# Kernel optimization log

Hardware: AMD Instinct MI355X
Metric: run time of the kernel (lower is better)

Reference implementation:

```python
import jax, jax.numpy as jnp
import numpy as np
import jax.scipy.linalg as jsl

# ---- module constants (mirror __init__ buffers) ----
T0, T1, DT = 0.0, 1.0, 1e-3
DIM, NSTEPS, M, TQ, B = 8, 2048, 64, 1024, 1
DS = (T1 - T0) / NSTEPS
STEPS = jnp.linspace(T0, T1, NSTEPS + 1)            # [S+1]
ZPTS = jnp.linspace(T0 + DT * 5.5, T1 - DT * 5.5, M)  # inducing points [M]
SQRT_DS = float(np.sqrt(DS))
SQRT_DT = float(np.sqrt(DT))


def _hurst(t, y0, W1, b1, W2, b2, Wc1, bc1, Wc2, bc2, dw, cw):
    # compute_hurst: sigmoid(driving_action(t)*dw + condition_net(y0)*cw)
    tc_in = t.reshape(-1, 1)                                             # [N,1]
    feat = jnp.concatenate([jnp.sin(tc_in), jnp.cos(tc_in), tc_in], -1)  # [N,3]
    tc = jax.nn.sigmoid(jnp.tanh(feat @ W1.T + b1) @ W2.T + b2)          # [N,dim]
    pc = jax.nn.sigmoid(jnp.tanh(y0 @ Wc1.T + bc1) @ Wc2.T + bc2)        # [1,dim]
    return jax.nn.sigmoid(tc * dw + pc * cw)                             # [N,dim]


def _safe_pow(x, a):
    # x**a for x>=0, with well-defined (zero) gradient at x==0
    mask = x > 0
    xs = jnp.where(mask, x, 1.0)
    return jnp.where(mask, xs ** a, 0.0)


def _compute_weight(t, y0, params, eps=1e-12):
    # compute_weight (Muniandy et al. weight); returns [S, N, dim]
    h = _hurst(t, y0, *params)[None]                              # [1,N,dim]
    d0 = jax.nn.relu(t[None, :] - STEPS[:-1, None])[..., None]    # [S,N,1]
    d1 = jax.nn.relu(t[None, :] - STEPS[1:, None])[..., None]     # [S,N,1]
    w = jnp.sqrt(_safe_pow(d0, 2.0 * h) - _safe_pow(d1, 2.0 * h) + eps)
    w = w / jnp.sqrt(2.0 * h * DS)
    return w / jnp.exp(jax.lax.lgamma(h + 0.5))


def _increment_weight(t, y0, params):
    # increment_weight: g_i / dt (finite difference of clamped weights)
    wa = jnp.maximum(_compute_weight(t, y0, params), 0.0)
    wb = jnp.maximum(_compute_weight(t + DT, y0, params), 0.0)
    return jnp.maximum((wb - wa) * SQRT_DS / DT, 0.0)             # [S,N,dim]


def _forward(t, y0, eps_z, W1, b1, W2, b2, Wc1, bc1, Wc2, bc2, dw, cw):
    params = (W1, b1, W2, b2, Wc1, bc1, Wc2, bc2, dw, cw)
    # --- precompute (inducing points) ---
    Kz = _increment_weight(ZPTS, y0, params)                # [S,M,dim]
    Kzz = jnp.einsum('smd,skd->dmk', Kz, Kz)                # [dim,M,M]
    Lz = jnp.linalg.cholesky(Kzz + 1e-6 * jnp.eye(M, dtype=Kzz.dtype))
    delta_Bz = jnp.einsum('dmk,dkb->dmb', Lz, eps_z)        # [dim,M,B]
    # --- forward (mean / sqrt(var)*sqrt(dt)) ---
    Kt = _increment_weight(t, y0, params)                   # [S,T,dim]
    Ktz = jnp.einsum('std,smd->dtm', Kt, Kz)                # [dim,T,M]
    alpha = jax.vmap(lambda L, b: jsl.cho_solve((L, True), b))(
        Lz, jnp.swapaxes(Ktz, -1, -2))                      # [dim,M,T]
    mean = jnp.einsum('dmt,dmb->dtb', alpha, delta_Bz)      # [dim,T,B]
    Ktt = jnp.einsum('std,sud->dtu', Kt, Kt)                # [dim,T,T]
    var = Ktt - jnp.einsum('dmt,dmu->dtu', alpha, alpha)    # [dim,T,T]
    std = jnp.sqrt(jnp.maximum(var, 1e-12)) * SQRT_DT
    return mean.reshape(-1, DIM), std.reshape(-1, DIM)


def setup_inputs() -> dict:
    key = jax.random.key(0)
    ks = jax.random.split(key, 12)
    return {
        't': jax.random.uniform(ks[0], (TQ,), jnp.float32, T0 + 0.05, T1 - 0.05),
        'y0': jax.random.normal(ks[1], (1, 1), jnp.float32),
        'eps_z': jax.random.normal(ks[2], (DIM, M, B), jnp.float32),
        'W1': jax.random.normal(ks[3], (10, 3), jnp.float32) * 0.3,
        'b1': jax.random.normal(ks[4], (10,), jnp.float32) * 0.1,
        'W2': jax.random.normal(ks[5], (DIM, 10), jnp.float32) * 0.3,
        'b2': jax.random.normal(ks[6], (DIM,), jnp.float32) * 0.1,
        'Wc1': jax.random.normal(ks[7], (10, 1), jnp.float32) * 0.3,
        'bc1': jax.random.normal(ks[8], (10,), jnp.float32) * 0.1,
        'Wc2': jax.random.normal(ks[9], (DIM, 10), jnp.float32) * 0.3,
        'bc2': jax.random.normal(ks[10], (DIM,), jnp.float32) * 0.1,
        'dw': jnp.array([0.5], jnp.float32),
        'cw': jnp.array([0.5], jnp.float32),
    }


def reference(t, y0, eps_z, W1, b1, W2, b2, Wc1, bc1, Wc2, bc2, dw, cw):
    return _forward(t, y0, eps_z, W1, b1, W2, b2, Wc1, bc1, Wc2, bc2, dw, cw)
```

## Files before the change

### kernel.cpp

```cpp
#include <hip/hip_runtime.h>
#include <cmath>

#define DIMN 8
#define SSTEPS 2048
#define MZ 64
#define TQN 1024
#define DS_F    4.8828125e-4f
#define DT_F    1.0e-3f
#define SCALE_F 22.09708691207961f
#define SQRTDT_F 0.031622776601683794f
#define LN2_F   0.6931471805599453f

typedef _Float16 f16x8 __attribute__((ext_vector_type(8)));
typedef float f32x4 __attribute__((ext_vector_type(4)));

__device__ __forceinline__ float sigmoidf_(float x) { return 1.f / (1.f + expf(-x)); }

__device__ __forceinline__ void gl_lds16(const _Float16* g, _Float16* l)
{
    __builtin_amdgcn_global_load_lds(
        (const __attribute__((address_space(1))) unsigned int*)g,
        (__attribute__((address_space(3))) unsigned int*)l, 16, 0, 0);
}

__global__ void coef_kernel(const float* __restrict__ t_in, const float* __restrict__ y0,
                            const float* __restrict__ W1, const float* __restrict__ b1,
                            const float* __restrict__ W2, const float* __restrict__ b2,
                            const float* __restrict__ Wc1, const float* __restrict__ bc1,
                            const float* __restrict__ Wc2, const float* __restrict__ bc2,
                            const float* __restrict__ dw, const float* __restrict__ cw,
                            float4* __restrict__ coef_t, float4* __restrict__ coef_z,
                            float* __restrict__ times_z)
{
    int gid = blockIdx.x * blockDim.x + threadIdx.x;
    if (gid >= TQN + MZ) return;
    bool isz = gid >= TQN;
    float tv;
    if (!isz) {
        tv = t_in[gid];
    } else {
        int j = gid - TQN;
        tv = 0.0055f + (float)j * (0.989f / 63.0f);
        times_z[j] = tv;
    }
    float y = y0[0];
    float hc[10];
    #pragma unroll
    for (int j = 0; j < 10; ++j) hc[j] = tanhf(y * Wc1[j] + bc1[j]);
    float pc[DIMN];
    #pragma unroll
    for (int d = 0; d < DIMN; ++d) {
        float s = bc2[d];
        #pragma unroll
        for (int j = 0; j < 10; ++j) s += hc[j] * Wc2[d * 10 + j];
        pc[d] = sigmoidf_(s);
    }
    float dww = dw[0], cww = cw[0];
    float4 outv[DIMN];
    for (int which = 0; which < 2; ++which) {
        float tt = (which == 0) ? tv : tv + DT_F;
        float st = sinf(tt), ct = cosf(tt);
        float hid[10];
        #pragma unroll
        for (int j = 0; j < 10; ++j)
            hid[j] = tanhf(st * W1[j * 3 + 0] + ct * W1[j * 3 + 1] + tt * W1[j * 3 + 2] + b1[j]);
        #pragma unroll
        for (int d = 0; d < DIMN; ++d) {
            float s = b2[d];
            #pragma unroll
            for (int j = 0; j < 10; ++j) s += hid[j] * W2[d * 10 + j];
            float tc = sigmoidf_(s);
            float h = sigmoidf_(tc * dww + pc[d] * cww);
            float e = 2.f * h;
            float c = rsqrtf(e * DS_F) / tgammaf(h + 0.5f);
            if (which == 0) { outv[d].x = e; outv[d].y = c; }
            else            { outv[d].z = e; outv[d].w = c; }
        }
    }
    float4* dst = isz ? (coef_z + (size_t)(gid - TQN) * DIMN) : (coef_t + (size_t)gid * DIMN);
    #pragma unroll
    for (int d = 0; d < DIMN; ++d) dst[d] = outv[d];
}

__device__ __forceinline__ void side_weights(float tt, float e, float c, int sbase,
                                             float (&w)[8])
{
    float xprev = tt - (float)sbase * DS_F;
    float pa = 0.f;
    if (xprev > 0.f) pa = __builtin_amdgcn_exp2f(e * __builtin_amdgcn_logf(xprev));
    #pragma unroll
    for (int k = 1; k <= 8; ++k) {
        float xk = tt - (float)(sbase + k) * DS_F;
        float D, pan;
        if (xk > 0.f) {
            float om = xk * __builtin_amdgcn_rcpf(xprev);
            float y2 = e * __builtin_amdgcn_logf(om);
            float wl = y2 * LN2_F;
            float em = wl * (1.f + wl * (0.5f + wl * (0.16666667f + wl * (0.041666668f + wl * 0.008333334f))));
            float g = -em;
            if (wl < -0.3f) g = 1.f - __builtin_amdgcn_exp2f(y2);
            D = pa * g;
            pan = pa - D;
        } else {
            D = pa;
            pan = 0.f;
        }
        w[k - 1] = __builtin_amdgcn_sqrtf(D + 1e-12f) * c;
        pa = pan;
        xprev = xk;
    }
}

__device__ __forceinline__ unsigned pack_hl(float v)
{
    _Float16 h = (_Float16)v;
    _Float16 l = (_Float16)(v - (float)h);
    unsigned short hu = __builtin_bit_cast(unsigned short, h);
    unsigned short lu = __builtin_bit_cast(unsigned short, l);
    return (unsigned)hu | ((unsigned)lu << 16);
}

__global__ __launch_bounds__(256) void kmat_t_kernel(const float* __restrict__ times,
                                                     const float4* __restrict__ coef,
                                                     _Float16* __restrict__ KThi,
                                                     _Float16* __restrict__ KTlo)
{
    int tid = threadIdx.x;
    int txx = tid & 31, sidx = tid >> 5;
    int t = blockIdx.x * 32 + txx;
    int sbase = blockIdx.y * 64 + sidx * 8;
    int d = blockIdx.z;
    __shared__ unsigned shhl[32][65];
    float tq = times[t];
    float4 cf = coef[(size_t)t * DIMN + d];
    float wa[8], wb[8];
    side_weights(tq,        cf.x, cf.y, sbase, wa);
    side_weights(tq + DT_F, cf.z, cf.w, sbase, wb);
    #pragma unroll
    for (int k = 0; k < 8; ++k) {
        float v = fmaxf(wb[k] - wa[k], 0.f) * SCALE_F;
        shhl[txx][sidx * 8 + k] = pack_hl(v);
    }
    __syncthreads();
    int tl = tid >> 3, sc = tid & 7;
    unsigned dwv[8];
    #pragma unroll
    for (int j = 0; j < 8; ++j) dwv[j] = shhl[tl][sc * 8 + j];
    uint4 hv, lv;
    hv.x = __builtin_amdgcn_perm(dwv[1], dwv[0], 0x05040100u);
    hv.y = __builtin_amdgcn_perm(dwv[3], dwv[2], 0x05040100u);
    hv.z = __builtin_amdgcn_perm(dwv[5], dwv[4], 0x05040100u);
    hv.w = __builtin_amdgcn_perm(dwv[7], dwv[6], 0x05040100u);
    lv.x = __builtin_amdgcn_perm(dwv[1], dwv[0], 0x07060302u);
    lv.y = __builtin_amdgcn_perm(dwv[3], dwv[2], 0x07060302u);
    lv.z = __builtin_amdgcn_perm(dwv[5], dwv[4], 0x07060302u);
    lv.w = __builtin_amdgcn_perm(dwv[7], dwv[6], 0x07060302u);
    size_t o = ((size_t)(d * 1024) + blockIdx.x * 32 + tl) * 2048 + blockIdx.y * 64 + sc * 8;
    *(uint4*)&KThi[o] = hv;
    *(uint4*)&KTlo[o] = lv;
}

__global__ __launch_bounds__(256) void kmat_z_kernel(const float* __restrict__ times,
                                                     const float4* __restrict__ coef,
                                                     float* __restrict__ Kz,
                                                     _Float16* __restrict__ KzThi,
                                                     _Float16* __restrict__ KzTlo)
{
    int tid = threadIdx.x;
    int txx = tid & 31, sidx = tid >> 5;
    int m = blockIdx.x * 32 + txx;
    int sbase = blockIdx.y * 64 + sidx * 8;
    int d = blockIdx.z;
    __shared__ unsigned shhl[32][65];
    float tq = times[m];
    float4 cf = coef[(size_t)m * DIMN + d];
    float wa[8], wb[8];
    side_weights(tq,        cf.x, cf.y, sbase, wa);
    side_weights(tq + DT_F, cf.z, cf.w, sbase, wb);
    #pragma unroll
    for (int k = 0; k < 8; ++k) {
        float v = fmaxf(wb[k] - wa[k], 0.f) * SCALE_F;
        Kz[((size_t)d * SSTEPS + sbase + k) * 64 + m] = v;
        shhl[txx][sidx * 8 + k] = pack_hl(v);
    }
    __syncthreads();
    int tl = tid >> 3, sc = tid & 7;
    unsigned dwv[8];
    #pragma unroll
    for (int j = 0; j < 8; ++j) dwv[j] = shhl[tl][sc * 8 + j];
    uint4 hv, lv;
    hv.x = __builtin_amdgcn_perm(dwv[1], dwv[0], 0x05040100u);
    hv.y = __builtin_amdgcn_perm(dwv[3], dwv[2], 0x05040100u);
    hv.z = __builtin_amdgcn_perm(dwv[5], dwv[4], 0x05040100u);
    hv.w = __builtin_amdgcn_perm(dwv[7], dwv[6], 0x05040100u);
    lv.x = __builtin_amdgcn_perm(dwv[1], dwv[0], 0x07060302u);
    lv.y = __builtin_amdgcn_perm(dwv[3], dwv[2], 0x07060302u);
    lv.z = __builtin_amdgcn_perm(dwv[5], dwv[4], 0x07060302u);
    lv.w = __builtin_amdgcn_perm(dwv[7], dwv[6], 0x07060302u);
    size_t o = ((size_t)(d * 64) + blockIdx.x * 32 + tl) * 2048 + blockIdx.y * 64 + sc * 8;
    *(uint4*)&KzThi[o] = hv;
    *(uint4*)&KzTlo[o] = lv;
}

__global__ __launch_bounds__(256) void kzz_partial_kernel(const float* __restrict__ Kz,
                                                          float* __restrict__ part)
{
    int kidx = blockIdx.x;
    int d = blockIdx.y;
    int tid = threadIdx.x, tx = tid & 15, ty = tid >> 4;
    __shared__ float As[32][64];
    float acc[4][4] = {};
    const float* base = Kz + ((size_t)d * SSTEPS + (size_t)kidx * 256) * 64;
    for (int c = 0; c < 8; ++c) {
        __syncthreads();
        #pragma unroll
        for (int l = 0; l < 2; ++l) {
            int idx = tid + l * 256;
            int r = idx >> 4, c4 = idx & 15;
            *(float4*)&As[r][c4 * 4] = *(const float4*)(base + (size_t)(c * 32 + r) * 64 + c4 * 4);
        }
        __syncthreads();
        #pragma unroll
        for (int k = 0; k < 32; ++k) {
            float av[4], bv[4];
            *(float4*)&av[0] = *(float4*)&As[k][ty * 4];
            *(float4*)&bv[0] = *(float4*)&As[k][tx * 4];
            #pragma unroll
            for (int i = 0; i < 4; ++i)
                #pragma unroll
                for (int j = 0; j < 4; ++j) acc[i][j] += av[i] * bv[j];
        }
    }
    float* dst = part + (size_t)(kidx * DIMN + d) * 4096;
    #pragma unroll
    for (int i = 0; i < 4; ++i)
        *(float4*)&dst[(size_t)(ty * 4 + i) * 64 + tx * 4] =
            make_float4(acc[i][0], acc[i][1], acc[i][2], acc[i][3]);
}

__global__ void reduce_kernel(const float* __restrict__ in, float* __restrict__ out,
                              int n, int parts)
{
    int i = blockIdx.x * 256 + threadIdx.x;
    if (i >= n) return;
    float s = 0.f;
    for (int p = 0; p < parts; ++p) s += in[(size_t)p * n + i];
    out[i] = s;
}

__global__ __launch_bounds__(64) void chol_kernel(const float* __restrict__ Kzz,
                                                  const float* __restrict__ eps_z,
                                                  float* __restrict__ Lz, float* __restrict__ dBz)
{
    int d = blockIdx.x, i = threadIdx.x;
    __shared__ float A[64][65];
    for (int r = 0; r < 64; ++r)
        A[r][i] = Kzz[(size_t)d * 4096 + (size_t)r * 64 + i] + ((r == i) ? 1e-6f : 0.f);
    __syncthreads();
    for (int j = 0; j < 64; ++j) {
        float s = 0.f;
        if (i >= j) {
            s = A[i][j];
            for (int k = 0; k < j; ++k) s -= A[i][k] * A[j][k];
        }
        __syncthreads();
        if (i == j) A[j][j] = sqrtf(fmaxf(s, 1e-30f));
        __syncthreads();
        if (i > j) A[i][j] = s / A[j][j];
        __syncthreads();
    }
    for (int r = 0; r < 64; ++r)
        Lz[(size_t)d * 4096 + (size_t)r * 64 + i] = (i <= r) ? A[r][i] : 0.f;
    float s = 0.f;
    for (int k = 0; k <= i; ++k) s += A[i][k] * eps_z[d * 64 + k];
    dBz[d * 64 + i] = s;
}

__global__ __launch_bounds__(256, 2) void ktz_mfma_kernel(const _Float16* __restrict__ KThi,
                                                          const _Float16* __restrict__ KTlo,
                                                          const _Float16* __restrict__ KzThi,
                                                          const _Float16* __restrict__ KzTlo,
                                                          float* __restrict__ part)
{
    int tid = threadIdx.x;
    int wave = tid >> 6, lane = tid & 63;
    int n = lane & 15, q = lane >> 4;
    int lr = lane >> 2, lc = (lane & 3) * 8;
    int d = blockIdx.x;
    int t0 = blockIdx.y * 128;
    int split = blockIdx.z;
    int wr = (wave >> 1) * 64, wc = (wave & 1) * 32;

    __shared__ _Float16 Ah[2][128][32], Al[2][128][32];
    __shared__ _Float16 Bh[2][64][32],  Bl[2][64][32];

    f32x4 acc[4][2];
    #pragma unroll
    for (int i = 0; i < 4; ++i)
        #pragma unroll
        for (int j = 0; j < 2; ++j) acc[i][j] = (f32x4)0.f;

    const size_t aRow = (size_t)(d * 1024 + t0);
    const size_t bRow = (size_t)(d * 64);
    int segA = wave * 32;
    int segB = wave * 16;

    auto stage = [&](int buf, int c) {
        int s0 = split * 512 + c * 32;
        size_t ga = (aRow + segA + lr) * 2048 + s0 + lc;
        size_t gb = (bRow + segB + lr) * 2048 + s0 + lc;
        gl_lds16(KThi + ga,               &Ah[buf][segA][0]);
        gl_lds16(KThi + ga + 16 * 2048,   &Ah[buf][segA + 16][0]);
        gl_lds16(KTlo + ga,               &Al[buf][segA][0]);
        gl_lds16(KTlo + ga + 16 * 2048,   &Al[buf][segA + 16][0]);
        gl_lds16(KzThi + gb,              &Bh[buf][segB][0]);
        gl_lds16(KzTlo + gb,              &Bl[buf][segB][0]);
    };

    stage(0, 0);
    __syncthreads();
    for (int c = 0; c < 16; ++c) {
        int buf = c & 1;
        if (c + 1 < 16) stage(buf ^ 1, c + 1);
        f16x8 fAh[4], fAl[4], fBh[2], fBl[2];
        #pragma unroll
        for (int i = 0; i < 4; ++i) {
            fAh[i] = *(f16x8*)&Ah[buf][wr + i * 16 + n][q * 8];
            fAl[i] = *(f16x8*)&Al[buf][wr + i * 16 + n][q * 8];
        }
        #pragma unroll
        for (int j = 0; j < 2; ++j) {
            fBh[j] = *(f16x8*)&Bh[buf][wc + j * 16 + n][q * 8];
            fBl[j] = *(f16x8*)&Bl[buf][wc + j * 16 + n][q * 8];
        }
        #pragma unroll
        for (int i = 0; i < 4; ++i)
            #pragma unroll
            for (int j = 0; j < 2; ++j) {
                acc[i][j] = __builtin_amdgcn_mfma_f32_16x16x32_f16(fAh[i], fBh[j], acc[i][j], 0, 0, 0);
                acc[i][j] = __builtin_amdgcn_mfma_f32_16x16x32_f16(fAh[i], fBl[j], acc[i][j], 0, 0, 0);
                acc[i][j] = __builtin_amdgcn_mfma_f32_16x16x32_f16(fAl[i], fBh[j], acc[i][j], 0, 0, 0);
            }
        __syncthreads();
    }
    float* dst = part + ((size_t)(split * DIMN + d)) * 1024 * 64;
    #pragma unroll
    for (int i = 0; i < 4; ++i)
        #pragma unroll
        for (int j = 0; j < 2; ++j)
            #pragma unroll
            for (int r = 0; r < 4; ++r) {
                int t = t0 + wr + i * 16 + q * 4 + r;
                dst[(size_t)t * 64 + wc + j * 16 + n] = acc[i][j][r];
            }
}

__global__ __launch_bounds__(64) void solve_kernel(const float* __restrict__ Lz,
                                                   const float* __restrict__ part2,
                                                   const float* __restrict__ dBz,
                                                   _Float16* __restrict__ aPhi,
                                                   _Float16* __restrict__ aPlo,
                                                   _Float16* __restrict__ aNhi,
                                                   _Float16* __restrict__ aNlo,
                                                   float* __restrict__ out0)
{
    int d = blockIdx.y;
    int t0 = blockIdx.x * 64;
    int i = threadIdx.x;
    __shared__ float L[64][65];
    __shared__ float bL[64][65];
    __shared__ float inv[64];
    __shared__ float dB[64];
    for (int r = 0; r < 64; ++r)
        L[r][i] = Lz[(size_t)d * 4096 + (size_t)r * 64 + i];
    dB[i] = dBz[d * 64 + i];
    for (int r = 0; r < 64; ++r) {
        size_t base = ((size_t)d * 1024 + t0 + r) * 64 + i;
        float s = part2[base] + part2[base + 524288] + part2[base + 1048576] + part2[base + 1572864];
        bL[i][r] = s;
    }
    __syncthreads();
    inv[i] = 1.f / L[i][i];
    __syncthreads();
    for (int j = 0; j < 64; ++j) {
        float s = bL[j][i];
        for (int k = 0; k < j; ++k) s -= L[j][k] * bL[k][i];
        bL[j][i] = s * inv[j];
    }
    for (int j = 63; j >= 0; --j) {
        float s = bL[j][i];
        for (int k = j + 1; k < 64; ++k) s -= L[k][j] * bL[k][i];
        bL[j][i] = s * inv[j];
    }
    float mn = 0.f;
    for (int m = 0; m < 64; ++m) mn += bL[m][i] * dB[m];
    out0[d * 1024 + t0 + i] = mn;
    size_t o = ((size_t)(d * 1024 + t0 + i)) * 64;
    for (int g = 0; g < 8; ++g) {
        union { _Float16 h[8]; float4 v; } ph, pl, nh, nl;
        #pragma unroll
        for (int k = 0; k < 8; ++k) {
            float x = bL[g * 8 + k][i];
            _Float16 h = (_Float16)x;
            _Float16 lo = (_Float16)(x - (float)h);
            ph.h[k] = h;  pl.h[k] = lo;
            nh.h[k] = -h; nl.h[k] = -lo;
        }
        *(float4*)&aPhi[o + g * 8] = ph.v;
        *(float4*)&aPlo[o + g * 8] = pl.v;
        *(float4*)&aNhi[o + g * 8] = nh.v;
        *(float4*)&aNlo[o + g * 8] = nl.v;
    }
}

__global__ __launch_bounds__(256, 2) void var_mfma_kernel(const _Float16* __restrict__ KThi,
                                                          const _Float16* __restrict__ KTlo,
                                                          const _Float16* __restrict__ aPhi,
                                                          const _Float16* __restrict__ aPlo,
                                                          const _Float16* __restrict__ aNhi,
                                                          const _Float16* __restrict__ aNlo,
                                                          float* __restrict__ out1)
{
    int tid = threadIdx.x;
    int wave = tid >> 6, lane = tid & 63;
    int n = lane & 15, q = lane >> 4;
    int lr = lane >> 2, lc = (lane & 3) * 8;
    int d = blockIdx.x;
    int t0 = blockIdx.y * 128, u0 = blockIdx.z * 128;
    int wr = (wave >> 1) * 64, wc = (wave & 1) * 64;

    __shared__ _Float16 Ah[2][128][32], Al[2][128][32], Bh[2][128][32], Bl[2][128][32];

    f32x4 acc[4][4];
    #pragma unroll
    for (int i = 0; i < 4; ++i)
        #pragma unroll
        for (int j = 0; j < 4; ++j) acc[i][j] = (f32x4)0.f;

    const size_t aRow = (size_t)(d * 1024 + t0);
    const size_t bRow = (size_t)(d * 1024 + u0);
    int segA = wave * 32;

    auto stage = [&](int buf, int ck) {
        const _Float16 *ph, *pl, *qh, *ql;
        size_t str; int col;
        if (ck < 64) { ph = KThi; pl = KTlo; qh = KThi; ql = KTlo; str = 2048; col = ck * 32; }
        else         { ph = aPhi; pl = aPlo; qh = aNhi; ql = aNlo; str = 64;  col = (ck - 64) * 32; }
        size_t ga = (aRow + segA + lr) * str + col + lc;
        size_t gb = (bRow + segA + lr) * str + col + lc;
        gl_lds16(ph + ga,            &Ah[buf][segA][0]);
        gl_lds16(ph + ga + 16 * str, &Ah[buf][segA + 16][0]);
        gl_lds16(pl + ga,            &Al[buf][segA][0]);
        gl_lds16(pl + ga + 16 * str, &Al[buf][segA + 16][0]);
        gl_lds16(qh + gb,            &Bh[buf][segA][0]);
        gl_lds16(qh + gb + 16 * str, &Bh[buf][segA + 16][0]);
        gl_lds16(ql + gb,            &Bl[buf][segA][0]);
        gl_lds16(ql + gb + 16 * str, &Bl[buf][segA + 16][0]);
    };

    stage(0, 0);
    __syncthreads();
    for (int ck = 0; ck < 66; ++ck) {
        int buf = ck & 1;
        if (ck + 1 < 66) stage(buf ^ 1, ck + 1);
        f16x8 fAh[4], fAl[4], fBh[4], fBl[4];
        #pragma unroll
        for (int i = 0; i < 4; ++i) {
            fAh[i] = *(f16x8*)&Ah[buf][wr + i * 16 + n][q * 8];
            fAl[i] = *(f16x8*)&Al[buf][wr + i * 16 + n][q * 8];
            fBh[i] = *(f16x8*)&Bh[buf][wc + i * 16 + n][q * 8];
            fBl[i] = *(f16x8*)&Bl[buf][wc + i * 16 + n][q * 8];
        }
        #pragma unroll
        for (int i = 0; i < 4; ++i)
            #pragma unroll
            for (int j = 0; j < 4; ++j) {
                acc[i][j] = __builtin_amdgcn_mfma_f32_16x16x32_f16(fAh[i], fBh[j], acc[i][j], 0, 0, 0);
                acc[i][j] = __builtin_amdgcn_mfma_f32_16x16x32_f16(fAh[i], fBl[j], acc[i][j], 0, 0, 0);
                acc[i][j] = __builtin_amdgcn_mfma_f32_16x16x32_f16(fAl[i], fBh[j], acc[i][j], 0, 0, 0);
            }
        __syncthreads();
    }
    float* dst = out1 + ((size_t)d << 20);
    #pragma unroll
    for (int i = 0; i < 4; ++i)
        #pragma unroll
        for (int j = 0; j < 4; ++j)
            #pragma unroll
            for (int r = 0; r < 4; ++r) {
                int t = t0 + wr + i * 16 + q * 4 + r;
                int u = u0 + wc + j * 16 + n;
                float v = acc[i][j][r];
                dst[(size_t)t * 1024 + u] = sqrtf(fmaxf(v, 1e-12f)) * SQRTDT_F;
            }
}

extern "C" void kernel_launch(void* const* d_in, const int* in_sizes, int n_in,
                              void* d_out, int out_size, void* d_ws, size_t ws_size,
                              hipStream_t stream)
{
    const float* t_in  = (const float*)d_in[0];
    const float* y0    = (const float*)d_in[1];
    const float* eps_z = (const float*)d_in[2];
    const float* W1    = (const float*)d_in[3];
    const float* b1    = (const float*)d_in[4];
    const float* W2    = (const float*)d_in[5];
    const float* b2    = (const float*)d_in[6];
    const float* Wc1   = (const float*)d_in[7];
    const float* bc1   = (const float*)d_in[8];
    const float* Wc2   = (const float*)d_in[9];
    const float* bc2   = (const float*)d_in[10];
    const float* dw    = (const float*)d_in[11];
    const float* cw    = (const float*)d_in[12];

    float* ws = (float*)d_ws;
    size_t off = 0;
    auto carve = [&](size_t n) { float* p = ws + off; off += n; return p; };
    float* coef_t   = carve(32768);
    float* coef_z   = carve(2048);
    float* times_z  = carve(64);
    float* Kzz      = carve(32768);
    float* Lz       = carve(32768);
    float* dBz      = carve(512);
    float* Kz       = carve(1048576);
    _Float16* KThi  = (_Float16*)carve(8388608);
    _Float16* KTlo  = (_Float16*)carve(8388608);
    _Float16* KzThi = (_Float16*)carve(524288);
    _Float16* KzTlo = (_Float16*)carve(524288);
    float* part1    = carve(262144);
    float* part2    = carve(2097152);
    _Float16* aPhi  = (_Float16*)carve(262144);
    _Float16* aPlo  = (_Float16*)carve(262144);
    _Float16* aNhi  = (_Float16*)carve(262144);
    _Float16* aNlo  = (_Float16*)carve(262144);

    float* out0 = (float*)d_out;
    float* out1 = out0 + (size_t)DIMN * 1024;

    coef_kernel<<<9, 128, 0, stream>>>(t_in, y0, W1, b1, W2, b2, Wc1, bc1, Wc2, bc2, dw, cw,
                                       (float4*)coef_t, (float4*)coef_z, times_z);
    kmat_t_kernel<<<dim3(32, 32, 8), 256, 0, stream>>>(t_in, (const float4*)coef_t,
                                                       KThi, KTlo);
    kmat_z_kernel<<<dim3(2, 32, 8), 256, 0, stream>>>(times_z, (const float4*)coef_z,
                                                      Kz, KzThi, KzTlo);
    kzz_partial_kernel<<<dim3(8, 8), 256, 0, stream>>>(Kz, part1);
    reduce_kernel<<<128, 256, 0, stream>>>(part1, Kzz, 32768, 8);
    chol_kernel<<<8, 64, 0, stream>>>(Kzz, eps_z, Lz, dBz);
    ktz_mfma_kernel<<<dim3(8, 8, 4), 256, 0, stream>>>(KThi, KTlo, KzThi, KzTlo, part2);
    solve_kernel<<<dim3(16, 8), 64, 0, stream>>>(Lz, part2, dBz, aPhi, aPlo, aNhi, aNlo, out0);
    var_mfma_kernel<<<dim3(8, 8, 8), 256, 0, stream>>>(KThi, KTlo, aPhi, aPlo, aNhi, aNlo, out1);
}
```

Baseline: 385.9 us.

## Skip zero weight strips, drop LDS transpose, load MFMA B operands directly to registers

```diff
diff --git a/kernel.cpp b/kernel.cpp
--- a/kernel.cpp
+++ b/kernel.cpp
@@ -111,53 +111,37 @@
     }
 }
 
-__device__ __forceinline__ unsigned pack_hl(float v)
-{
-    _Float16 h = (_Float16)v;
-    _Float16 l = (_Float16)(v - (float)h);
-    unsigned short hu = __builtin_bit_cast(unsigned short, h);
-    unsigned short lu = __builtin_bit_cast(unsigned short, l);
-    return (unsigned)hu | ((unsigned)lu << 16);
-}
-
 __global__ __launch_bounds__(256) void kmat_t_kernel(const float* __restrict__ times,
                                                      const float4* __restrict__ coef,
                                                      _Float16* __restrict__ KThi,
                                                      _Float16* __restrict__ KTlo)
 {
     int tid = threadIdx.x;
-    int txx = tid & 31, sidx = tid >> 5;
-    int t = blockIdx.x * 32 + txx;
-    int sbase = blockIdx.y * 64 + sidx * 8;
+    int strip = tid & 63, tloc = tid >> 6;
+    int t = blockIdx.x * 4 + tloc;
+    int sbase = blockIdx.y * 512 + strip * 8;
     int d = blockIdx.z;
-    __shared__ unsigned shhl[32][65];
     float tq = times[t];
+    size_t o = ((size_t)(d * 1024) + t) * 2048 + sbase;
+    if (tq + DT_F <= (float)sbase * DS_F) {
+        *(uint4*)&KThi[o] = make_uint4(0u, 0u, 0u, 0u);
+        *(uint4*)&KTlo[o] = make_uint4(0u, 0u, 0u, 0u);
+        return;
+    }
     float4 cf = coef[(size_t)t * DIMN + d];
     float wa[8], wb[8];
     side_weights(tq,        cf.x, cf.y, sbase, wa);
     side_weights(tq + DT_F, cf.z, cf.w, sbase, wb);
+    union { _Float16 h[8]; uint4 v; } hv, lv;
     #pragma unroll
     for (int k = 0; k < 8; ++k) {
         float v = fmaxf(wb[k] - wa[k], 0.f) * SCALE_F;
-        shhl[txx][sidx * 8 + k] = pack_hl(v);
-    }
-    __syncthreads();
-    int tl = tid >> 3, sc = tid & 7;
-    unsigned dwv[8];
-    #pragma unroll
-    for (int j = 0; j < 8; ++j) dwv[j] = shhl[tl][sc * 8 + j];
-    uint4 hv, lv;
-    hv.x = __builtin_amdgcn_perm(dwv[1], dwv[0], 0x05040100u);
-    hv.y = __builtin_amdgcn_perm(dwv[3], dwv[2], 0x05040100u);
-    hv.z = __builtin_amdgcn_perm(dwv[5], dwv[4], 0x05040100u);
-    hv.w = __builtin_amdgcn_perm(dwv[7], dwv[6], 0x05040100u);
-    lv.x = __builtin_amdgcn_perm(dwv[1], dwv[0], 0x07060302u);
-    lv.y = __builtin_amdgcn_perm(dwv[3], dwv[2], 0x07060302u);
-    lv.z = __builtin_amdgcn_perm(dwv[5], dwv[4], 0x07060302u);
-    lv.w = __builtin_amdgcn_perm(dwv[7], dwv[6], 0x07060302u);
-    size_t o = ((size_t)(d * 1024) + blockIdx.x * 32 + tl) * 2048 + blockIdx.y * 64 + sc * 8;
-    *(uint4*)&KThi[o] = hv;
-    *(uint4*)&KTlo[o] = lv;
+        _Float16 h = (_Float16)v;
+        hv.h[k] = h;
+        lv.h[k] = (_Float16)(v - (float)h);
+    }
+    *(uint4*)&KThi[o] = hv.v;
+    *(uint4*)&KTlo[o] = lv.v;
 }
 
 __global__ __launch_bounds__(256) void kmat_z_kernel(const float* __restrict__ times,
@@ -167,39 +151,35 @@
                                                      _Float16* __restrict__ KzTlo)
 {
     int tid = threadIdx.x;
-    int txx = tid & 31, sidx = tid >> 5;
-    int m = blockIdx.x * 32 + txx;
-    int sbase = blockIdx.y * 64 + sidx * 8;
+    int strip = tid & 63, tloc = tid >> 6;
+    int m = blockIdx.x * 4 + tloc;
+    int sbase = blockIdx.y * 512 + strip * 8;
     int d = blockIdx.z;
-    __shared__ unsigned shhl[32][65];
     float tq = times[m];
+    size_t o = ((size_t)(d * 64) + m) * 2048 + sbase;
+    if (tq + DT_F <= (float)sbase * DS_F) {
+        *(uint4*)&KzThi[o] = make_uint4(0u, 0u, 0u, 0u);
+        *(uint4*)&KzTlo[o] = make_uint4(0u, 0u, 0u, 0u);
+        #pragma unroll
+        for (int k = 0; k < 8; ++k)
+            Kz[((size_t)d * SSTEPS + sbase + k) * 64 + m] = 0.f;
+        return;
+    }
     float4 cf = coef[(size_t)m * DIMN + d];
     float wa[8], wb[8];
     side_weights(tq,        cf.x, cf.y, sbase, wa);
     side_weights(tq + DT_F, cf.z, cf.w, sbase, wb);
+    union { _Float16 h[8]; uint4 v; } hv, lv;
     #pragma unroll
     for (int k = 0; k < 8; ++k) {
         float v = fmaxf(wb[k] - wa[k], 0.f) * SCALE_F;
         Kz[((size_t)d * SSTEPS + sbase + k) * 64 + m] = v;
-        shhl[txx][sidx * 8 + k] = pack_hl(v);
-    }
-    __syncthreads();
-    int tl = tid >> 3, sc = tid & 7;
-    unsigned dwv[8];
-    #pragma unroll
-    for (int j = 0; j < 8; ++j) dwv[j] = shhl[tl][sc * 8 + j];
-    uint4 hv, lv;
-    hv.x = __builtin_amdgcn_perm(dwv[1], dwv[0], 0x05040100u);
-    hv.y = __builtin_amdgcn_perm(dwv[3], dwv[2], 0x05040100u);
-    hv.z = __builtin_amdgcn_perm(dwv[5], dwv[4], 0x05040100u);
-    hv.w = __builtin_amdgcn_perm(dwv[7], dwv[6], 0x05040100u);
-    lv.x = __builtin_amdgcn_perm(dwv[1], dwv[0], 0x07060302u);
-    lv.y = __builtin_amdgcn_perm(dwv[3], dwv[2], 0x07060302u);
-    lv.z = __builtin_amdgcn_perm(dwv[5], dwv[4], 0x07060302u);
-    lv.w = __builtin_amdgcn_perm(dwv[7], dwv[6], 0x07060302u);
-    size_t o = ((size_t)(d * 64) + blockIdx.x * 32 + tl) * 2048 + blockIdx.y * 64 + sc * 8;
-    *(uint4*)&KzThi[o] = hv;
-    *(uint4*)&KzTlo[o] = lv;
+        _Float16 h = (_Float16)v;
+        hv.h[k] = h;
+        lv.h[k] = (_Float16)(v - (float)h);
+    }
+    *(uint4*)&KzThi[o] = hv.v;
+    *(uint4*)&KzTlo[o] = lv.v;
 }
 
 __global__ __launch_bounds__(256) void kzz_partial_kernel(const float* __restrict__ Kz,
@@ -292,7 +272,6 @@
     int wr = (wave >> 1) * 64, wc = (wave & 1) * 32;
 
     __shared__ _Float16 Ah[2][128][32], Al[2][128][32];
-    __shared__ _Float16 Bh[2][64][32],  Bl[2][64][32];
 
     f32x4 acc[4][2];
     #pragma unroll
@@ -301,47 +280,52 @@
         for (int j = 0; j < 2; ++j) acc[i][j] = (f32x4)0.f;
 
     const size_t aRow = (size_t)(d * 1024 + t0);
-    const size_t bRow = (size_t)(d * 64);
     int segA = wave * 32;
-    int segB = wave * 16;
-
-    auto stage = [&](int buf, int c) {
-        int s0 = split * 512 + c * 32;
-        size_t ga = (aRow + segA + lr) * 2048 + s0 + lc;
-        size_t gb = (bRow + segB + lr) * 2048 + s0 + lc;
-        gl_lds16(KThi + ga,               &Ah[buf][segA][0]);
-        gl_lds16(KThi + ga + 16 * 2048,   &Ah[buf][segA + 16][0]);
-        gl_lds16(KTlo + ga,               &Al[buf][segA][0]);
-        gl_lds16(KTlo + ga + 16 * 2048,   &Al[buf][segA + 16][0]);
-        gl_lds16(KzThi + gb,              &Bh[buf][segB][0]);
-        gl_lds16(KzTlo + gb,              &Bl[buf][segB][0]);
+
+    auto stageA = [&](int buf, int c) {
+        size_t ga = (aRow + segA + lr) * 2048 + (size_t)(split * 512 + c * 32) + lc;
+        gl_lds16(KThi + ga,             &Ah[buf][segA][0]);
+        gl_lds16(KThi + ga + 16 * 2048, &Ah[buf][segA + 16][0]);
+        gl_lds16(KTlo + ga,             &Al[buf][segA][0]);
+        gl_lds16(KTlo + ga + 16 * 2048, &Al[buf][segA + 16][0]);
     };
-
-    stage(0, 0);
+    auto loadB = [&](int c, f16x8* Bh_, f16x8* Bl_) {
+        #pragma unroll
+        for (int j = 0; j < 2; ++j) {
+            size_t off = (size_t)(d * 64 + wc + j * 16 + n) * 2048
+                       + (size_t)(split * 512 + c * 32) + q * 8;
+            Bh_[j] = *(const f16x8*)(KzThi + off);
+            Bl_[j] = *(const f16x8*)(KzTlo + off);
+        }
+    };
+
+    f16x8 cBh[2], cBl[2], nBh[2], nBl[2];
+    loadB(0, cBh, cBl);
+    stageA(0, 0);
     __syncthreads();
     for (int c = 0; c < 16; ++c) {
         int buf = c & 1;
-        if (c + 1 < 16) stage(buf ^ 1, c + 1);
-        f16x8 fAh[4], fAl[4], fBh[2], fBl[2];
+        if (c + 1 < 16) {
+            loadB(c + 1, nBh, nBl);
+            stageA(buf ^ 1, c + 1);
+        }
+        f16x8 fAh[4], fAl[4];
         #pragma unroll
         for (int i = 0; i < 4; ++i) {
             fAh[i] = *(f16x8*)&Ah[buf][wr + i * 16 + n][q * 8];
             fAl[i] = *(f16x8*)&Al[buf][wr + i * 16 + n][q * 8];
         }
         #pragma unroll
-        for (int j = 0; j < 2; ++j) {
-            fBh[j] = *(f16x8*)&Bh[buf][wc + j * 16 + n][q * 8];
-            fBl[j] = *(f16x8*)&Bl[buf][wc + j * 16 + n][q * 8];
-        }
-        #pragma unroll
         for (int i = 0; i < 4; ++i)
             #pragma unroll
             for (int j = 0; j < 2; ++j) {
-                acc[i][j] = __builtin_amdgcn_mfma_f32_16x16x32_f16(fAh[i], fBh[j], acc[i][j], 0, 0, 0);
-                acc[i][j] = __builtin_amdgcn_mfma_f32_16x16x32_f16(fAh[i], fBl[j], acc[i][j], 0, 0, 0);
-                acc[i][j] = __builtin_amdgcn_mfma_f32_16x16x32_f16(fAl[i], fBh[j], acc[i][j], 0, 0, 0);
+                acc[i][j] = __builtin_amdgcn_mfma_f32_16x16x32_f16(fAh[i], cBh[j], acc[i][j], 0, 0, 0);
+                acc[i][j] = __builtin_amdgcn_mfma_f32_16x16x32_f16(fAh[i], cBl[j], acc[i][j], 0, 0, 0);
+                acc[i][j] = __builtin_amdgcn_mfma_f32_16x16x32_f16(fAl[i], cBh[j], acc[i][j], 0, 0, 0);
             }
         __syncthreads();
+        #pragma unroll
+        for (int j = 0; j < 2; ++j) { cBh[j] = nBh[j]; cBl[j] = nBl[j]; }
     }
     float* dst = part + ((size_t)(split * DIMN + d)) * 1024 * 64;
     #pragma unroll
@@ -429,7 +413,7 @@
     int t0 = blockIdx.y * 128, u0 = blockIdx.z * 128;
     int wr = (wave >> 1) * 64, wc = (wave & 1) * 64;
 
-    __shared__ _Float16 Ah[2][128][32], Al[2][128][32], Bh[2][128][32], Bl[2][128][32];
+    __shared__ _Float16 Ah[2][128][32], Al[2][128][32];
 
     f32x4 acc[4][4];
     #pragma unroll
@@ -441,45 +425,66 @@
     const size_t bRow = (size_t)(d * 1024 + u0);
     int segA = wave * 32;
 
-    auto stage = [&](int buf, int ck) {
-        const _Float16 *ph, *pl, *qh, *ql;
-        size_t str; int col;
-        if (ck < 64) { ph = KThi; pl = KTlo; qh = KThi; ql = KTlo; str = 2048; col = ck * 32; }
-        else         { ph = aPhi; pl = aPlo; qh = aNhi; ql = aNlo; str = 64;  col = (ck - 64) * 32; }
-        size_t ga = (aRow + segA + lr) * str + col + lc;
-        size_t gb = (bRow + segA + lr) * str + col + lc;
-        gl_lds16(ph + ga,            &Ah[buf][segA][0]);
-        gl_lds16(ph + ga + 16 * str, &Ah[buf][segA + 16][0]);
-        gl_lds16(pl + ga,            &Al[buf][segA][0]);
-        gl_lds16(pl + ga + 16 * str, &Al[buf][segA + 16][0]);
-        gl_lds16(qh + gb,            &Bh[buf][segA][0]);
-        gl_lds16(qh + gb + 16 * str, &Bh[buf][segA + 16][0]);
-        gl_lds16(ql + gb,            &Bl[buf][segA][0]);
-        gl_lds16(ql + gb + 16 * str, &Bl[buf][segA + 16][0]);
+    auto stageA = [&](int buf, int ck) {
+        if (ck < 64) {
+            size_t ga = (aRow + segA + lr) * 2048 + (size_t)(ck * 32) + lc;
+            gl_lds16(KThi + ga,             &Ah[buf][segA][0]);
+            gl_lds16(KThi + ga + 16 * 2048, &Ah[buf][segA + 16][0]);
+            gl_lds16(KTlo + ga,             &Al[buf][segA][0]);
+            gl_lds16(KTlo + ga + 16 * 2048, &Al[buf][segA + 16][0]);
+        } else {
+            size_t ga = (aRow + segA + lr) * 64 + (size_t)((ck - 64) * 32) + lc;
+            gl_lds16(aPhi + ga,           &Ah[buf][segA][0]);
+            gl_lds16(aPhi + ga + 16 * 64, &Ah[buf][segA + 16][0]);
+            gl_lds16(aPlo + ga,           &Al[buf][segA][0]);
+            gl_lds16(aPlo + ga + 16 * 64, &Al[buf][segA + 16][0]);
+        }
     };
-
-    stage(0, 0);
+    auto loadB = [&](int ck, f16x8* Bh_, f16x8* Bl_) {
+        if (ck < 64) {
+            #pragma unroll
+            for (int j = 0; j < 4; ++j) {
+                size_t off = (bRow + wc + j * 16 + n) * 2048 + (size_t)(ck * 32) + q * 8;
+                Bh_[j] = *(const f16x8*)(KThi + off);
+                Bl_[j] = *(const f16x8*)(KTlo + off);
+            }
+        } else {
+            #pragma unroll
+            for (int j = 0; j < 4; ++j) {
+                size_t off = (bRow + wc + j * 16 + n) * 64 + (size_t)((ck - 64) * 32) + q * 8;
+                Bh_[j] = *(const f16x8*)(aNhi + off);
+                Bl_[j] = *(const f16x8*)(aNlo + off);
+            }
+        }
+    };
+
+    f16x8 cBh[4], cBl[4], nBh[4], nBl[4];
+    loadB(0, cBh, cBl);
+    stageA(0, 0);
     __syncthreads();
     for (int ck = 0; ck < 66; ++ck) {
         int buf = ck & 1;
-        if (ck + 1 < 66) stage(buf ^ 1, ck + 1);
-        f16x8 fAh[4], fAl[4], fBh[4], fBl[4];
+        if (ck + 1 < 66) {
+            loadB(ck + 1, nBh, nBl);
+            stageA(buf ^ 1, ck + 1);
+        }
+        f16x8 fAh[4], fAl[4];
         #pragma unroll
         for (int i = 0; i < 4; ++i) {
             fAh[i] = *(f16x8*)&Ah[buf][wr + i * 16 + n][q * 8];
             fAl[i] = *(f16x8*)&Al[buf][wr + i * 16 + n][q * 8];
-            fBh[i] = *(f16x8*)&Bh[buf][wc + i * 16 + n][q * 8];
-            fBl[i] = *(f16x8*)&Bl[buf][wc + i * 16 + n][q * 8];
         }
         #pragma unroll
         for (int i = 0; i < 4; ++i)
             #pragma unroll
             for (int j = 0; j < 4; ++j) {
-                acc[i][j] = __builtin_amdgcn_mfma_f32_16x16x32_f16(fAh[i], fBh[j], acc[i][j], 0, 0, 0);
-                acc[i][j] = __builtin_amdgcn_mfma_f32_16x16x32_f16(fAh[i], fBl[j], acc[i][j], 0, 0, 0);
-                acc[i][j] = __builtin_amdgcn_mfma_f32_16x16x32_f16(fAl[i], fBh[j], acc[i][j], 0, 0, 0);
+                acc[i][j] = __builtin_amdgcn_mfma_f32_16x16x32_f16(fAh[i], cBh[j], acc[i][j], 0, 0, 0);
+                acc[i][j] = __builtin_amdgcn_mfma_f32_16x16x32_f16(fAh[i], cBl[j], acc[i][j], 0, 0, 0);
+                acc[i][j] = __builtin_amdgcn_mfma_f32_16x16x32_f16(fAl[i], cBh[j], acc[i][j], 0, 0, 0);
             }
         __syncthreads();
+        #pragma unroll
+        for (int j = 0; j < 4; ++j) { cBh[j] = nBh[j]; cBl[j] = nBl[j]; }
     }
     float* dst = out1 + ((size_t)d << 20);
     #pragma unroll
@@ -539,9 +544,9 @@
 
     coef_kernel<<<9, 128, 0, stream>>>(t_in, y0, W1, b1, W2, b2, Wc1, bc1, Wc2, bc2, dw, cw,
                                        (float4*)coef_t, (float4*)coef_z, times_z);
-    kmat_t_kernel<<<dim3(32, 32, 8), 256, 0, stream>>>(t_in, (const float4*)coef_t,
+    kmat_t_kernel<<<dim3(256, 4, 8), 256, 0, stream>>>(t_in, (const float4*)coef_t,
                                                        KThi, KTlo);
-    kmat_z_kernel<<<dim3(2, 32, 8), 256, 0, stream>>>(times_z, (const float4*)coef_z,
+    kmat_z_kernel<<<dim3(16, 4, 8), 256, 0, stream>>>(times_z, (const float4*)coef_z,
                                                       Kz, KzThi, KzTlo);
     kzz_partial_kernel<<<dim3(8, 8), 256, 0, stream>>>(Kz, part1);
     reduce_kernel<<<128, 256, 0, stream>>>(part1, Kzz, 32768, 8);
```

After: 544.4 us. +41.1%, slower.
